# Optimization experiments

Hardware: AMD Instinct MI355X
Metric: run time of the kernel (lower is better)

## Reference

```python
import jax, jax.numpy as jnp
import numpy as np

M, H = 7, 200                 # ensemble size, hidden width
OBS, ACT = 32, 8
C = OBS + ACT                 # model input dim
DOUT = OBS + 1                # next-obs delta + reward
N = 100000                    # number of transitions
E_NUM = 5                     # number of elites
MAX_LOGVAR, MIN_LOGVAR = 0.5, -10.0
REWARD_SCALE, REWARD_BIAS = 1.0, 0.0
TERM_THRESH = 50.0


def setup_inputs() -> dict:
    key = jax.random.key(0)
    ks = jax.random.split(key, 10)
    def w(k, shape, fan_in):
        return jax.random.normal(k, shape, jnp.float32) / np.float32(np.sqrt(fan_in))
    return {
        "observations": jax.random.normal(ks[0], (N, OBS), jnp.float32),
        "actions": jax.random.normal(ks[1], (N, ACT), jnp.float32),
        "scaler_mu": jax.random.normal(ks[2], (C,), jnp.float32) * 0.1,
        "scaler_std": jax.random.uniform(ks[3], (C,), jnp.float32, 0.5, 1.5),
        "W1": w(ks[4], (M, C, H), C), "b1": jnp.zeros((M, 1, H), jnp.float32),
        "W2": w(ks[5], (M, H, H), H), "b2": jnp.zeros((M, 1, H), jnp.float32),
        "W3": w(ks[6], (M, H, H), H), "b3": jnp.zeros((M, 1, H), jnp.float32),
        "W4": w(ks[7], (M, H, 2 * DOUT), H), "b4": jnp.zeros((M, 1, 2 * DOUT), jnp.float32),
        "elites": jnp.arange(E_NUM, dtype=jnp.int32),
    }


def _ensemble_mlp(z, W1, b1, W2, b2, W3, b3, W4, b4):
    # z: [M, R, C] -> mean, logvar: [M, R, DOUT]
    h = jax.nn.swish(jnp.einsum('mrc,mch->mrh', z, W1) + b1)
    h = jax.nn.swish(jnp.einsum('mrh,mhk->mrk', h, W2) + b2)
    h = jax.nn.swish(jnp.einsum('mrh,mhk->mrk', h, W3) + b3)
    out = jnp.einsum('mrh,mhk->mrk', h, W4) + b4
    mean, logvar = out[..., :DOUT], out[..., DOUT:]
    logvar = MAX_LOGVAR - jax.nn.softplus(MAX_LOGVAR - logvar)
    logvar = MIN_LOGVAR + jax.nn.softplus(logvar - MIN_LOGVAR)
    return mean, logvar


def _terminal_fn(observations, actions, next_obs):
    # simple environment-style terminal predicate, shape [N, 1]
    return jnp.linalg.norm(next_obs, axis=-1, keepdims=True) > TERM_THRESH


def reference(observations, actions, scaler_mu, scaler_std,
              W1, b1, W2, b2, W3, b3, W4, b4, elites):
    key = jax.random.key(0)  # source uses the SAME key for permutation and noise
    z = jnp.concatenate([observations, actions], axis=1)
    z = (z - scaler_mu) / scaler_std
    n, c = z.shape
    e = elites.shape[0]
    r = (n - 1) // e + 1
    pad = e * r - n
    z = jnp.concatenate([z, jnp.zeros((pad, c), z.dtype)], axis=0)
    idxs = jax.random.permutation(key, e * r)
    tmp = z[idxs].reshape(e, r, c)                    # dispatch to elite slots
    zf = jnp.zeros((M, r, c), z.dtype).at[elites].set(tmp)
    mean, logvar = _ensemble_mlp(zf, W1, b1, W2, b2, W3, b3, W4, b4)
    std = jnp.exp(0.5 * logvar)
    ensemble_samples = mean + jax.random.normal(key, mean.shape) * std
    res = ensemble_samples[elites].reshape(e * r, DOUT)   # gather elites back
    es = jnp.zeros((e * r, DOUT), res.dtype).at[idxs].set(res)[:n]  # inverse perm
    samples = jnp.concatenate([es[:, :-1] + observations, es[:, -1:]], axis=1)
    next_obs = samples[..., :-1]
    reward = samples[..., -1] * REWARD_SCALE + REWARD_BIAS
    terminal = _terminal_fn(observations, actions, next_obs).squeeze(1)
    return next_obs, reward, terminal
```

## Files before the change

### kernel.cpp

```cpp
#include <hip/hip_runtime.h>
#include <stdint.h>

#define N_TOT   100000
#define NPAD    100352
#define NBLK    196
#define EPB     512
#define HISTN   (NBLK * 256)
#define R_PER   20000
#define NOISE_HALF 2310000u
#define PERM_HALF  50000u

#define JAX_PARTITIONABLE 1

#define ROWS 32
#define RG_N 2
#define BPM  625
#define MLP_GRID (5 * BPM)
#define KST  200

#define L1_U4 1664
#define L2_U4 5824
#define L4_U4 2240
#define PM_U4 (L1_U4 + 2 * L2_U4 + L4_U4)
#define L1OFF 0
#define L2OFF L1_U4
#define L3OFF (L1_U4 + L2_U4)
#define L4OFF (L1_U4 + 2 * L2_U4)
#define WPACK_BLOCKS 304

using f32x4  = __attribute__((ext_vector_type(4))) float;
using bf16x8 = __attribute__((ext_vector_type(8))) short;

__host__ __device__ __forceinline__ uint32_t rotl32(uint32_t x, unsigned d) {
  return (x << d) | (x >> (32u - d));
}

__host__ __device__ inline void tf2x32(uint32_t k0, uint32_t k1,
                                       uint32_t x0, uint32_t x1,
                                       uint32_t& o0, uint32_t& o1) {
  uint32_t k2 = k0 ^ k1 ^ 0x1BD11BDAu;
  x0 += k0; x1 += k1;
#define TFR(R) { x0 += x1; x1 = rotl32(x1, R); x1 ^= x0; }
  TFR(13u) TFR(15u) TFR(26u) TFR(6u)
  x0 += k1; x1 += k2 + 1u;
  TFR(17u) TFR(29u) TFR(16u) TFR(24u)
  x0 += k2; x1 += k0 + 2u;
  TFR(13u) TFR(15u) TFR(26u) TFR(6u)
  x0 += k0; x1 += k1 + 3u;
  TFR(17u) TFR(29u) TFR(16u) TFR(24u)
  x0 += k1; x1 += k2 + 4u;
  TFR(13u) TFR(15u) TFR(26u) TFR(6u)
  x0 += k2; x1 += k0 + 5u;
#undef TFR
  o0 = x0; o1 = x1;
}

__host__ __device__ inline uint32_t jax_bits32(uint32_t k0, uint32_t k1,
                                               uint32_t idx, uint32_t half) {
#if JAX_PARTITIONABLE
  (void)half;
  uint32_t o0, o1; tf2x32(k0, k1, 0u, idx, o0, o1);
  return o0 ^ o1;
#else
  uint32_t o0, o1;
  if (idx < half) { tf2x32(k0, k1, idx, idx + half, o0, o1); return o0; }
  else            { tf2x32(k0, k1, idx - half, idx, o0, o1); return o1; }
#endif
}

static void jax_split_host(uint32_t k0, uint32_t k1,
                           uint32_t* nk, uint32_t* sk) {
#if JAX_PARTITIONABLE
  tf2x32(k0, k1, 0u, 0u, nk[0], nk[1]);
  tf2x32(k0, k1, 0u, 1u, sk[0], sk[1]);
#else
  uint32_t a0, a1, b0, b1;
  tf2x32(k0, k1, 0u, 2u, a0, a1);
  tf2x32(k0, k1, 1u, 3u, b0, b1);
  nk[0] = a0; nk[1] = b0;
  sk[0] = a1; sk[1] = b1;
#endif
}

__device__ __forceinline__ void split2(float e0, float e1,
                                       uint32_t& hi, uint32_t& lo) {
  uint32_t u0 = __float_as_uint(e0), u1 = __float_as_uint(e1);
  float f0 = __uint_as_float(u0 & 0xFFFF0000u);
  float f1 = __uint_as_float(u1 & 0xFFFF0000u);
  uint32_t l0 = __float_as_uint(e0 - f0) >> 16;
  uint32_t l1 = __float_as_uint(e1 - f1) >> 16;
  hi = (u1 & 0xFFFF0000u) | (u0 >> 16);
  lo = (l1 << 16) | l0;
}

__device__ __forceinline__ void split1(float x, unsigned short& h,
                                       unsigned short& l) {
  uint32_t u = __float_as_uint(x);
  float fh = __uint_as_float(u & 0xFFFF0000u);
  h = (unsigned short)(u >> 16);
  l = (unsigned short)(__float_as_uint(x - fh) >> 16);
}

__device__ __forceinline__ float rec1(unsigned short h, unsigned short l) {
  return __uint_as_float((uint32_t)h << 16) + __uint_as_float((uint32_t)l << 16);
}

__device__ __forceinline__ bf16x8 punu4(uint4 x) {
  union { uint4 u; bf16x8 v; } t;
  t.u = x;
  return t.v;
}

__global__ __launch_bounds__(256) void k_pre(uint32_t kk0, uint32_t kk1,
                                             uint32_t* __restrict__ keys,
                                             uint32_t* __restrict__ vals,
                                             uint32_t* __restrict__ hist,
                                             uint32_t* __restrict__ histZ,
                                             const float* __restrict__ W1,
                                             const float* __restrict__ W2,
                                             const float* __restrict__ W3,
                                             const float* __restrict__ W4,
                                             uint4* __restrict__ wpH,
                                             uint4* __restrict__ wpL) {
  __shared__ uint32_t h[256];
  int tid = threadIdx.x;
  if (blockIdx.x < NBLK) {
    int b = blockIdx.x;
    h[tid] = 0;
    __syncthreads();
    uint32_t base = b * (uint32_t)EPB + tid * 2u;
    uint32_t kq[2], vq[2];
#pragma unroll
    for (int j = 0; j < 2; ++j) {
      uint32_t i = base + j;
      if (i < (uint32_t)N_TOT) {
        kq[j] = jax_bits32(kk0, kk1, i, PERM_HALF);
        vq[j] = i;
      } else {
        kq[j] = 0xFFFFFFFFu;
        vq[j] = 0xFFFFFFFFu;
      }
      atomicAdd(&h[kq[j] & 255u], 1u);
    }
    *(uint2*)(keys + base) = make_uint2(kq[0], kq[1]);
    *(uint2*)(vals + base) = make_uint2(vq[0], vq[1]);
    __syncthreads();
    hist[b * 256 + tid] = h[tid];
    histZ[b * 256 + tid] = 0;
  } else {
    int flat = (blockIdx.x - NBLK) * 256 + tid;
    if (flat >= 5 * PM_U4) return;
    int m = flat / PM_U4;
    int rem = flat - m * PM_U4;
    const float* W; int KIN, KOUT, nch, loc;
    if (rem < L2OFF)      { W = W1 + (size_t)m * 40 * 200;  KIN = 40;  KOUT = 200; nch = 2; loc = rem; }
    else if (rem < L3OFF) { W = W2 + (size_t)m * 200 * 200; KIN = 200; KOUT = 200; nch = 7; loc = rem - L2OFF; }
    else if (rem < L4OFF) { W = W3 + (size_t)m * 200 * 200; KIN = 200; KOUT = 200; nch = 7; loc = rem - L3OFF; }
    else                  { W = W4 + (size_t)m * 200 * 66;  KIN = 200; KOUT = 66;  nch = 7; loc = rem - L4OFF; }
    int lane = loc & 63;
    int tc = loc >> 6;
    int ch = tc % nch;
    int t  = tc / nch;
    int g = lane >> 4, cr = lane & 15;
    int k0 = ch * 32 + g * 8;
    int col = t * 16 + cr;
    const bool ok = (k0 < KIN) && (col < KOUT);
    float w[8];
#pragma unroll
    for (int j = 0; j < 8; ++j)
      w[j] = ok ? W[(size_t)(k0 + j) * KOUT + col] : 0.f;
    uint32_t hi[4], lo[4];
#pragma unroll
    for (int d = 0; d < 4; ++d)
      split2(w[2 * d], w[2 * d + 1], hi[d], lo[d]);
    wpH[flat] = make_uint4(hi[0], hi[1], hi[2], hi[3]);
    wpL[flat] = make_uint4(lo[0], lo[1], lo[2], lo[3]);
  }
}

template<bool GENNEXT, bool LAST>
__global__ __launch_bounds__(512) void k_scat(const uint32_t* __restrict__ keyIn,
                                              const uint32_t* __restrict__ valIn,
                                              uint32_t* __restrict__ keyOut,
                                              uint32_t* __restrict__ valOut,
                                              const uint32_t* __restrict__ histRaw,
                                              uint32_t* __restrict__ histNext,
                                              uint32_t* __restrict__ histZero,
                                              int shift, uint32_t nk0, uint32_t nk1) {
  __shared__ uint32_t ptot[2][256];
  __shared__ uint32_t pbef[2][256];
  __shared__ uint32_t tot[256];
  __shared__ uint32_t bas[256];
  __shared__ uint32_t offD[256];
  __shared__ uint32_t dig[EPB];
  __shared__ uint32_t histc[8 * 256];
  const int b = blockIdx.x, tid = threadIdx.x;

  const uint32_t key = keyIn[b * EPB + tid];
  const uint32_t val = valIn[b * EPB + tid];

  {
    const int d8 = tid & 255;
    const int half = tid >> 8;
    uint32_t t = 0, before = 0;
    const int b0 = half * (NBLK / 2);
    for (int b2 = b0; b2 < b0 + NBLK / 2; ++b2) {
      uint32_t v2 = histRaw[b2 * 256 + d8];
      t += v2;
      before += (b2 < b) ? v2 : 0u;
    }
    ptot[half][d8] = t;
    pbef[half][d8] = before;
    __syncthreads();
    if (tid < 256) {
      uint32_t tt = ptot[0][tid] + ptot[1][tid];
      tot[tid] = tt;
      bas[tid] = tt;
    }
    __syncthreads();
    for (int off = 1; off < 256; off <<= 1) {
      uint32_t v = 0;
      if (tid < 256 && tid >= off) v = bas[tid - off];
      __syncthreads();
      if (tid < 256) bas[tid] += v;
      __syncthreads();
    }
    if (tid < 256)
      offD[tid] = bas[tid] - tot[tid] + pbef[0][tid] + pbef[1][tid];
  }

  const uint32_t d = (key >> shift) & 255u;
  const int cp = tid >> 6;
  for (int x = tid; x < 8 * 256; x += EPB) histc[x] = 0;
  __syncthreads();
  dig[tid] = d;
  atomicAdd(&histc[cp * 256 + d], 1u);
  __syncthreads();
  if (tid < 256) {
    uint32_t run = 0;
#pragma unroll
    for (int c = 0; c < 8; ++c) {
      uint32_t t = histc[c * 256 + tid];
      histc[c * 256 + tid] = run;
      run += t;
    }
  }
  __syncthreads();
  int c = 0;
  for (int p = cp * 64; p < tid; ++p)
    c += (dig[p] == d);
  const uint32_t rank = histc[cp * 256 + d] + (uint32_t)c;
  const uint32_t off = offD[d] + rank;
  valOut[off] = val;
  if (!LAST) {
    uint32_t nkey;
    int nshift;
    if (GENNEXT) {
      nkey = (off < (uint32_t)N_TOT) ? jax_bits32(nk0, nk1, off, PERM_HALF)
                                     : 0xFFFFFFFFu;
      nshift = 0;
    } else {
      nkey = key;
      nshift = shift + 8;
    }
    keyOut[off] = nkey;
    atomicAdd(&histNext[(off / EPB) * 256 + ((nkey >> nshift) & 255u)], 1u);
    if (tid < 256) histZero[b * 256 + tid] = 0;
  }
}

__device__ inline float softplusf(float x) {
  float ax = fabsf(x);
  float r = log1pf(expf(-ax));
  return (x > 0.f) ? x + r : r;
}

__device__ inline float erfinvf_approx(float x) {
  float w = -logf((1.0f - x) * (1.0f + x));
  float p;
  if (w < 5.0f) {
    w = w - 2.5f;
    p = 2.81022636e-08f;
    p = fmaf(p, w, 3.43273939e-07f);
    p = fmaf(p, w, -3.5233877e-06f);
    p = fmaf(p, w, -4.39150654e-06f);
    p = fmaf(p, w, 0.00021858087f);
    p = fmaf(p, w, -0.00125372503f);
    p = fmaf(p, w, -0.00417768164f);
    p = fmaf(p, w, 0.246640727f);
    p = fmaf(p, w, 1.50140941f);
  } else {
    w = sqrtf(w) - 3.0f;
    p = -0.000200214257f;
    p = fmaf(p, w, 0.000100950558f);
    p = fmaf(p, w, 0.00134934322f);
    p = fmaf(p, w, -0.00367342844f);
    p = fmaf(p, w, 0.00573950773f);
    p = fmaf(p, w, -0.0076224613f);
    p = fmaf(p, w, 0.00943887047f);
    p = fmaf(p, w, 1.00167406f);
    p = fmaf(p, w, 2.83297682f);
  }
  return p * x;
}

template<int KOUT, int NTILES, int NCH, bool ACTV>
__device__ __forceinline__ void layer_mfma(unsigned short* __restrict__ Ahi,
                                           unsigned short* __restrict__ Alo,
                                           const uint4* __restrict__ wpH,
                                           const uint4* __restrict__ wpL,
                                           int woff,
                                           const float* __restrict__ bm,
                                           int wv, int lane) {
  constexpr int MAXT = (NTILES + 3) / 4;
  const int g  = lane >> 4;
  const int cr = lane & 15;
  f32x4 acc[RG_N][MAXT];
#pragma unroll
  for (int rg = 0; rg < RG_N; ++rg)
#pragma unroll
    for (int ti = 0; ti < MAXT; ++ti)
      acc[rg][ti] = (f32x4){0.f, 0.f, 0.f, 0.f};

  for (int ch = 0; ch < NCH; ++ch) {
    const int k0 = ch * 32 + g * 8;
    const bool ok = (k0 + 8 <= KST);
    const int ka = ok ? k0 : 0;
    uint4 hfa[RG_N], lfa[RG_N];
#pragma unroll
    for (int rg = 0; rg < RG_N; ++rg) {
      uint4 h = *(const uint4*)(Ahi + (rg * 16 + cr) * KST + ka);
      uint4 l = *(const uint4*)(Alo + (rg * 16 + cr) * KST + ka);
      if (!ok) { h = make_uint4(0, 0, 0, 0); l = make_uint4(0, 0, 0, 0); }
      hfa[rg] = h; lfa[rg] = l;
    }
#pragma unroll
    for (int ti = 0; ti < MAXT; ++ti) {
      const int t = wv + ti * 4;
      if (t < NTILES) {
        const int idx = woff + (t * NCH + ch) * 64 + lane;
        bf16x8 vbh = punu4(wpH[idx]);
        bf16x8 vbl = punu4(wpL[idx]);
#pragma unroll
        for (int rg = 0; rg < RG_N; ++rg) {
          bf16x8 vah = punu4(hfa[rg]);
          bf16x8 val = punu4(lfa[rg]);
          acc[rg][ti] = __builtin_amdgcn_mfma_f32_16x16x32_bf16(vah, vbh, acc[rg][ti], 0, 0, 0);
          acc[rg][ti] = __builtin_amdgcn_mfma_f32_16x16x32_bf16(val, vbh, acc[rg][ti], 0, 0, 0);
          acc[rg][ti] = __builtin_amdgcn_mfma_f32_16x16x32_bf16(vah, vbl, acc[rg][ti], 0, 0, 0);
        }
      }
    }
  }
  __syncthreads();
#pragma unroll
  for (int ti = 0; ti < MAXT; ++ti) {
    const int t = wv + ti * 4;
    if (t < NTILES) {
      const int col = t * 16 + cr;
      if (col < KOUT) {
        const float bias = bm[col];
#pragma unroll
        for (int rg = 0; rg < RG_N; ++rg) {
#pragma unroll
          for (int rr = 0; rr < 4; ++rr) {
            float x = acc[rg][ti][rr] + bias;
            if (ACTV) x = x / (1.0f + expf(-x));
            unsigned short h, l;
            split1(x, h, l);
            const int row = rg * 16 + g * 4 + rr;
            Ahi[row * KST + col] = h;
            Alo[row * KST + col] = l;
          }
        }
      }
    }
  }
  __syncthreads();
}

__global__ __launch_bounds__(256, 6) void k_mlp(
    const float* __restrict__ obs, const float* __restrict__ act,
    const float* __restrict__ mu, const float* __restrict__ sst,
    const uint4* __restrict__ wpH, const uint4* __restrict__ wpL,
    const float* __restrict__ b1, const float* __restrict__ b2,
    const float* __restrict__ b3, const float* __restrict__ b4,
    const uint32_t* __restrict__ idxs, float* __restrict__ outv) {
  __shared__ __align__(16) unsigned short Ahi[ROWS * KST];
  __shared__ __align__(16) unsigned short Alo[ROWS * KST];
  __shared__ uint32_t jrow[ROWS];
  __shared__ float nrm[ROWS];
  __shared__ float muv[40];
  __shared__ float rsd[40];
  const int tid = threadIdx.x;
  const int m  = blockIdx.x / BPM;
  const int bb = blockIdx.x - m * BPM;
  const int i0 = m * R_PER + bb * ROWS;
  const int wv = tid >> 6;
  const int lane = tid & 63;
  const int mw = m * PM_U4;

  if (tid < ROWS) {
    jrow[tid] = idxs[i0 + tid];
    nrm[tid] = 0.f;
  }
  if (tid >= 64 && tid < 104) {
    int cc = tid - 64;
    muv[cc] = mu[cc];
    rsd[cc] = 1.0f / sst[cc];
  }
  __syncthreads();

  for (int t = tid; t < ROWS * 64; t += 256) {
    int rr = t >> 6, cc = t & 63;
    float v = 0.f;
    if (cc < 40) {
      uint32_t j = jrow[rr];
      float x = (cc < 32) ? obs[(size_t)j * 32 + cc] : act[(size_t)j * 8 + (cc - 32)];
      v = (x - muv[cc]) * rsd[cc];
    }
    unsigned short h, l;
    split1(v, h, l);
    Ahi[rr * KST + cc] = h;
    Alo[rr * KST + cc] = l;
  }
  __syncthreads();

  layer_mfma<200, 13, 2, true >(Ahi, Alo, wpH, wpL, mw + L1OFF, b1 + (size_t)m * 200, wv, lane);
  layer_mfma<200, 13, 7, true >(Ahi, Alo, wpH, wpL, mw + L2OFF, b2 + (size_t)m * 200, wv, lane);
  layer_mfma<200, 13, 7, true >(Ahi, Alo, wpH, wpL, mw + L3OFF, b3 + (size_t)m * 200, wv, lane);
  layer_mfma< 66,  5, 7, false>(Ahi, Alo, wpH, wpL, mw + L4OFF, b4 + (size_t)m * 66, wv, lane);

  float* onext = outv;
  float* orew  = outv + 3200000;
  float* oterm = outv + 3300000;

  for (int t = tid; t < ROWS * 33; t += 256) {
    int rw = t / 33, kc = t - rw * 33;
    float mean = rec1(Ahi[rw * KST + kc],      Alo[rw * KST + kc]);
    float lvr  = rec1(Ahi[rw * KST + 33 + kc], Alo[rw * KST + 33 + kc]);
    float lv = 0.5f - softplusf(0.5f - lvr);
    lv = -10.0f + softplusf(lv + 10.0f);
    float sd = expf(0.5f * lv);
    int q = bb * ROWS + rw;
    uint32_t tno = (uint32_t)(m * 660000 + q * 33 + kc);
    uint32_t bits = jax_bits32(0u, 0u, tno, NOISE_HALF);
    float f = __uint_as_float((bits >> 9) | 0x3F800000u) - 1.0f;
    const float LOu = -0.99999994f;
    float u = fmaxf(LOu, fmaf(f, 2.0f, LOu));
    float nz = 1.41421356237f * erfinvf_approx(u);
    float s = mean + nz * sd;
    uint32_t j = jrow[rw];
    if (kc < 32) {
      float no = s + obs[(size_t)j * 32 + kc];
      onext[(size_t)j * 32 + kc] = no;
      atomicAdd(&nrm[rw], no * no);
    } else {
      orew[j] = s;
    }
  }
  __syncthreads();
  if (tid < ROWS) {
    uint32_t j = jrow[tid];
    oterm[j] = (sqrtf(nrm[tid]) > 50.0f) ? 1.0f : 0.0f;
  }
}

extern "C" void kernel_launch(void* const* d_in, const int* in_sizes, int n_in,
                              void* d_out, int out_size, void* d_ws, size_t ws_size,
                              hipStream_t stream) {
  (void)in_sizes; (void)n_in; (void)out_size; (void)ws_size;
  const float* obs = (const float*)d_in[0];
  const float* act = (const float*)d_in[1];
  const float* mu  = (const float*)d_in[2];
  const float* sst = (const float*)d_in[3];
  const float* W1  = (const float*)d_in[4];
  const float* b1  = (const float*)d_in[5];
  const float* W2  = (const float*)d_in[6];
  const float* b2  = (const float*)d_in[7];
  const float* W3  = (const float*)d_in[8];
  const float* b3  = (const float*)d_in[9];
  const float* W4  = (const float*)d_in[10];
  const float* b4  = (const float*)d_in[11];

  uint8_t* ws = (uint8_t*)d_ws;
  uint32_t* keysA = (uint32_t*)(ws);
  uint32_t* keysB = (uint32_t*)(ws + 401408);
  uint32_t* valsA = (uint32_t*)(ws + 802816);
  uint32_t* valsB = (uint32_t*)(ws + 1204224);
  uint32_t* hA    = (uint32_t*)(ws + 1605632);
  uint32_t* hB    = (uint32_t*)(ws + 1806336);
  uint32_t* hC    = (uint32_t*)(ws + 2007040);
  uint4*    wpH   = (uint4*)(ws + 2207744);
  uint4*    wpL   = (uint4*)(ws + 3451904);

  uint32_t key0[2] = {0u, 0u}, key1[2], sub1[2], key2[2], sub2[2];
  jax_split_host(key0[0], key0[1], key1, sub1);
  jax_split_host(key1[0], key1[1], key2, sub2);

  dim3 g(NBLK), blk(256), blk512(512);

  k_pre<<<dim3(NBLK + WPACK_BLOCKS), blk, 0, stream>>>(sub1[0], sub1[1],
      keysA, valsA, hA, hB, W1, W2, W3, W4, wpH, wpL);
  k_scat<false,false><<<g, blk512, 0, stream>>>(keysA, valsA, keysB, valsB, hA, hB, hC, 0,  0u, 0u);
  k_scat<false,false><<<g, blk512, 0, stream>>>(keysB, valsB, keysA, valsA, hB, hC, hA, 8,  0u, 0u);
  k_scat<false,false><<<g, blk512, 0, stream>>>(keysA, valsA, keysB, valsB, hC, hA, hB, 16, 0u, 0u);
  k_scat<true, false><<<g, blk512, 0, stream>>>(keysB, valsB, keysA, valsA, hA, hB, hC, 24, sub2[0], sub2[1]);
  k_scat<false,false><<<g, blk512, 0, stream>>>(keysA, valsA, keysB, valsB, hB, hC, hA, 0,  0u, 0u);
  k_scat<false,false><<<g, blk512, 0, stream>>>(keysB, valsB, keysA, valsA, hC, hA, hB, 8,  0u, 0u);
  k_scat<false,false><<<g, blk512, 0, stream>>>(keysA, valsA, keysB, valsB, hA, hB, hC, 16, 0u, 0u);
  k_scat<false,true ><<<g, blk512, 0, stream>>>(keysB, valsB, keysA, valsA, hB, hC, hA, 24, 0u, 0u);

  k_mlp<<<dim3(MLP_GRID), blk, 0, stream>>>(obs, act, mu, sst,
                                            wpH, wpL, b1, b2, b3, b4,
                                            valsA, (float*)d_out);
}
```

Measured before the change: 302.4 us.

## Spread weight packing across radix-sort scatter passes and use fast reciprocal in swish

Moves the bf16 hi/lo weight-packing work out of the key-generation kernel and spreads it over extra blocks in each of the eight radix scatter launches. The aim is to shorten the critical first kernel and hide packing behind latency-bound sort passes. It also swaps the division in swish for a v_rcp_f32 reciprocal, which lowers ALU cost in the MLP epilogue but gives slightly less accurate results.

```diff
diff --git a/kernel.cpp b/kernel.cpp
--- a/kernel.cpp
+++ b/kernel.cpp
@@ -26,7 +26,7 @@
 #define L2OFF L1_U4
 #define L3OFF (L1_U4 + L2_U4)
 #define L4OFF (L1_U4 + 2 * L2_U4)
-#define WPACK_BLOCKS 304
+#define WPB   19
 
 using f32x4  = __attribute__((ext_vector_type(4))) float;
 using bf16x8 = __attribute__((ext_vector_type(8))) short;
@@ -111,71 +111,75 @@
   return t.v;
 }
 
+__device__ __forceinline__ float fast_rcp(float x) {
+  float r;
+  asm("v_rcp_f32 %0, %1" : "=v"(r) : "v"(x));
+  return r;
+}
+
+__device__ __forceinline__ void wpack_one(int flat,
+                                          const float* __restrict__ W1,
+                                          const float* __restrict__ W2,
+                                          const float* __restrict__ W3,
+                                          const float* __restrict__ W4,
+                                          uint4* __restrict__ wpH,
+                                          uint4* __restrict__ wpL) {
+  int m = flat / PM_U4;
+  int rem = flat - m * PM_U4;
+  const float* W; int KIN, KOUT, nch, loc;
+  if (rem < L2OFF)      { W = W1 + (size_t)m * 40 * 200;  KIN = 40;  KOUT = 200; nch = 2; loc = rem; }
+  else if (rem < L3OFF) { W = W2 + (size_t)m * 200 * 200; KIN = 200; KOUT = 200; nch = 7; loc = rem - L2OFF; }
+  else if (rem < L4OFF) { W = W3 + (size_t)m * 200 * 200; KIN = 200; KOUT = 200; nch = 7; loc = rem - L3OFF; }
+  else                  { W = W4 + (size_t)m * 200 * 66;  KIN = 200; KOUT = 66;  nch = 7; loc = rem - L4OFF; }
+  int lane = loc & 63;
+  int tc = loc >> 6;
+  int ch = tc % nch;
+  int t  = tc / nch;
+  int g = lane >> 4, cr = lane & 15;
+  int k0 = ch * 32 + g * 8;
+  int col = t * 16 + cr;
+  const bool ok = (k0 < KIN) && (col < KOUT);
+  float w[8];
+#pragma unroll
+  for (int j = 0; j < 8; ++j)
+    w[j] = ok ? W[(size_t)(k0 + j) * KOUT + col] : 0.f;
+  uint32_t hi[4], lo[4];
+#pragma unroll
+  for (int d = 0; d < 4; ++d)
+    split2(w[2 * d], w[2 * d + 1], hi[d], lo[d]);
+  wpH[flat] = make_uint4(hi[0], hi[1], hi[2], hi[3]);
+  wpL[flat] = make_uint4(lo[0], lo[1], lo[2], lo[3]);
+}
+
 __global__ __launch_bounds__(256) void k_pre(uint32_t kk0, uint32_t kk1,
                                              uint32_t* __restrict__ keys,
                                              uint32_t* __restrict__ vals,
                                              uint32_t* __restrict__ hist,
-                                             uint32_t* __restrict__ histZ,
-                                             const float* __restrict__ W1,
-                                             const float* __restrict__ W2,
-                                             const float* __restrict__ W3,
-                                             const float* __restrict__ W4,
-                                             uint4* __restrict__ wpH,
-                                             uint4* __restrict__ wpL) {
+                                             uint32_t* __restrict__ histZ) {
   __shared__ uint32_t h[256];
   int tid = threadIdx.x;
-  if (blockIdx.x < NBLK) {
-    int b = blockIdx.x;
-    h[tid] = 0;
-    __syncthreads();
-    uint32_t base = b * (uint32_t)EPB + tid * 2u;
-    uint32_t kq[2], vq[2];
-#pragma unroll
-    for (int j = 0; j < 2; ++j) {
-      uint32_t i = base + j;
-      if (i < (uint32_t)N_TOT) {
-        kq[j] = jax_bits32(kk0, kk1, i, PERM_HALF);
-        vq[j] = i;
-      } else {
-        kq[j] = 0xFFFFFFFFu;
-        vq[j] = 0xFFFFFFFFu;
-      }
-      atomicAdd(&h[kq[j] & 255u], 1u);
-    }
-    *(uint2*)(keys + base) = make_uint2(kq[0], kq[1]);
-    *(uint2*)(vals + base) = make_uint2(vq[0], vq[1]);
-    __syncthreads();
-    hist[b * 256 + tid] = h[tid];
-    histZ[b * 256 + tid] = 0;
-  } else {
-    int flat = (blockIdx.x - NBLK) * 256 + tid;
-    if (flat >= 5 * PM_U4) return;
-    int m = flat / PM_U4;
-    int rem = flat - m * PM_U4;
-    const float* W; int KIN, KOUT, nch, loc;
-    if (rem < L2OFF)      { W = W1 + (size_t)m * 40 * 200;  KIN = 40;  KOUT = 200; nch = 2; loc = rem; }
-    else if (rem < L3OFF) { W = W2 + (size_t)m * 200 * 200; KIN = 200; KOUT = 200; nch = 7; loc = rem - L2OFF; }
-    else if (rem < L4OFF) { W = W3 + (size_t)m * 200 * 200; KIN = 200; KOUT = 200; nch = 7; loc = rem - L3OFF; }
-    else                  { W = W4 + (size_t)m * 200 * 66;  KIN = 200; KOUT = 66;  nch = 7; loc = rem - L4OFF; }
-    int lane = loc & 63;
-    int tc = loc >> 6;
-    int ch = tc % nch;
-    int t  = tc / nch;
-    int g = lane >> 4, cr = lane & 15;
-    int k0 = ch * 32 + g * 8;
-    int col = t * 16 + cr;
-    const bool ok = (k0 < KIN) && (col < KOUT);
-    float w[8];
-#pragma unroll
-    for (int j = 0; j < 8; ++j)
-      w[j] = ok ? W[(size_t)(k0 + j) * KOUT + col] : 0.f;
-    uint32_t hi[4], lo[4];
-#pragma unroll
-    for (int d = 0; d < 4; ++d)
-      split2(w[2 * d], w[2 * d + 1], hi[d], lo[d]);
-    wpH[flat] = make_uint4(hi[0], hi[1], hi[2], hi[3]);
-    wpL[flat] = make_uint4(lo[0], lo[1], lo[2], lo[3]);
-  }
+  int b = blockIdx.x;
+  h[tid] = 0;
+  __syncthreads();
+  uint32_t base = b * (uint32_t)EPB + tid * 2u;
+  uint32_t kq[2], vq[2];
+#pragma unroll
+  for (int j = 0; j < 2; ++j) {
+    uint32_t i = base + j;
+    if (i < (uint32_t)N_TOT) {
+      kq[j] = jax_bits32(kk0, kk1, i, PERM_HALF);
+      vq[j] = i;
+    } else {
+      kq[j] = 0xFFFFFFFFu;
+      vq[j] = 0xFFFFFFFFu;
+    }
+    atomicAdd(&h[kq[j] & 255u], 1u);
+  }
+  *(uint2*)(keys + base) = make_uint2(kq[0], kq[1]);
+  *(uint2*)(vals + base) = make_uint2(vq[0], vq[1]);
+  __syncthreads();
+  hist[b * 256 + tid] = h[tid];
+  histZ[b * 256 + tid] = 0;
 }
 
 template<bool GENNEXT, bool LAST>
@@ -186,7 +190,14 @@
                                               const uint32_t* __restrict__ histRaw,
                                               uint32_t* __restrict__ histNext,
                                               uint32_t* __restrict__ histZero,
-                                              int shift, uint32_t nk0, uint32_t nk1) {
+                                              int shift, uint32_t nk0, uint32_t nk1,
+                                              int wpass,
+                                              const float* __restrict__ W1,
+                                              const float* __restrict__ W2,
+                                              const float* __restrict__ W3,
+                                              const float* __restrict__ W4,
+                                              uint4* __restrict__ wpH,
+                                              uint4* __restrict__ wpL) {
   __shared__ uint32_t ptot[2][256];
   __shared__ uint32_t pbef[2][256];
   __shared__ uint32_t tot[256];
@@ -195,6 +206,13 @@
   __shared__ uint32_t dig[EPB];
   __shared__ uint32_t histc[8 * 256];
   const int b = blockIdx.x, tid = threadIdx.x;
+
+  if (b >= NBLK) {
+    int flat = (wpass * WPB + (b - NBLK)) * EPB + tid;
+    if (flat < 5 * PM_U4)
+      wpack_one(flat, W1, W2, W3, W4, wpH, wpL);
+    return;
+  }
 
   const uint32_t key = keyIn[b * EPB + tid];
   const uint32_t val = valIn[b * EPB + tid];
@@ -365,7 +383,7 @@
 #pragma unroll
           for (int rr = 0; rr < 4; ++rr) {
             float x = acc[rg][ti][rr] + bias;
-            if (ACTV) x = x / (1.0f + expf(-x));
+            if (ACTV) x = x * fast_rcp(1.0f + expf(-x));
             unsigned short h, l;
             split1(x, h, l);
             const int row = rg * 16 + g * 4 + rr;
@@ -498,18 +516,17 @@
   jax_split_host(key0[0], key0[1], key1, sub1);
   jax_split_host(key1[0], key1[1], key2, sub2);
 
-  dim3 g(NBLK), blk(256), blk512(512);
-
-  k_pre<<<dim3(NBLK + WPACK_BLOCKS), blk, 0, stream>>>(sub1[0], sub1[1],
-      keysA, valsA, hA, hB, W1, W2, W3, W4, wpH, wpL);
-  k_scat<false,false><<<g, blk512, 0, stream>>>(keysA, valsA, keysB, valsB, hA, hB, hC, 0,  0u, 0u);
-  k_scat<false,false><<<g, blk512, 0, stream>>>(keysB, valsB, keysA, valsA, hB, hC, hA, 8,  0u, 0u);
-  k_scat<false,false><<<g, blk512, 0, stream>>>(keysA, valsA, keysB, valsB, hC, hA, hB, 16, 0u, 0u);
-  k_scat<true, false><<<g, blk512, 0, stream>>>(keysB, valsB, keysA, valsA, hA, hB, hC, 24, sub2[0], sub2[1]);
-  k_scat<false,false><<<g, blk512, 0, stream>>>(keysA, valsA, keysB, valsB, hB, hC, hA, 0,  0u, 0u);
-  k_scat<false,false><<<g, blk512, 0, stream>>>(keysB, valsB, keysA, valsA, hC, hA, hB, 8,  0u, 0u);
-  k_scat<false,false><<<g, blk512, 0, stream>>>(keysA, valsA, keysB, valsB, hA, hB, hC, 16, 0u, 0u);
-  k_scat<false,true ><<<g, blk512, 0, stream>>>(keysB, valsB, keysA, valsA, hB, hC, hA, 24, 0u, 0u);
+  dim3 gs(NBLK + WPB), blk(256), blk512(512);
+
+  k_pre<<<dim3(NBLK), blk, 0, stream>>>(sub1[0], sub1[1], keysA, valsA, hA, hB);
+  k_scat<false,false><<<gs, blk512, 0, stream>>>(keysA, valsA, keysB, valsB, hA, hB, hC, 0,  0u, 0u, 0, W1, W2, W3, W4, wpH, wpL);
+  k_scat<false,false><<<gs, blk512, 0, stream>>>(keysB, valsB, keysA, valsA, hB, hC, hA, 8,  0u, 0u, 1, W1, W2, W3, W4, wpH, wpL);
+  k_scat<false,false><<<gs, blk512, 0, stream>>>(keysA, valsA, keysB, valsB, hC, hA, hB, 16, 0u, 0u, 2, W1, W2, W3, W4, wpH, wpL);
+  k_scat<true, false><<<gs, blk512, 0, stream>>>(keysB, valsB, keysA, valsA, hA, hB, hC, 24, sub2[0], sub2[1], 3, W1, W2, W3, W4, wpH, wpL);
+  k_scat<false,false><<<gs, blk512, 0, stream>>>(keysA, valsA, keysB, valsB, hB, hC, hA, 0,  0u, 0u, 4, W1, W2, W3, W4, wpH, wpL);
+  k_scat<false,false><<<gs, blk512, 0, stream>>>(keysB, valsB, keysA, valsA, hC, hA, hB, 8,  0u, 0u, 5, W1, W2, W3, W4, wpH, wpL);
+  k_scat<false,false><<<gs, blk512, 0, stream>>>(keysA, valsA, keysB, valsB, hA, hB, hC, 16, 0u, 0u, 6, W1, W2, W3, W4, wpH, wpL);
+  k_scat<false,true ><<<gs, blk512, 0, stream>>>(keysB, valsB, keysA, valsA, hB, hC, hA, 24, 0u, 0u, 7, W1, W2, W3, W4, wpH, wpL);
 
   k_mlp<<<dim3(MLP_GRID), blk, 0, stream>>>(obs, act, mu, sst,
                                             wpH, wpL, b1, b2, b3, b4,
```

New measurement: 303.0 us, median of 2. Within noise of the previous version (+0.2%).
